# Performance work log

Hardware: AMD Instinct MI355X
Metric: run time of the kernel (lower is better)

Reference implementation:

```python
import jax, jax.numpy as jnp
import numpy as np

K_NEIGHBORS = 5
EPS = 1e-12  # torch F.normalize eps


def _l2_normalize(x):
    n = jnp.linalg.norm(x, axis=-1, keepdims=True)
    return x / jnp.maximum(n, EPS)


def setup_inputs() -> dict:
    key = jax.random.key(0)
    k1, k2, k3, k4 = jax.random.split(key, 4)
    B, D = 256, 512
    N, A = 50000, 8
    return {
        "z_flowed": jax.random.normal(k1, (B, D), dtype=jnp.float32),
        "target_attrs": jax.random.randint(k2, (B, A), 0, 3, dtype=jnp.int32),
        "train_embeddings": jax.random.normal(k3, (N, D), dtype=jnp.float32),
        "train_attributes": jax.random.randint(k4, (N, A), 0, 3, dtype=jnp.int32),
    }


def reference(z_flowed, target_attrs, train_embeddings, train_attributes):
    B = z_flowed.shape[0]
    A = target_attrs.shape[1]
    z_norm = _l2_normalize(z_flowed)          # [B, D]
    train_norm = _l2_normalize(train_embeddings)  # [N, D]

    # batched attribute match: [B, N] count of matching attributes
    match_score = (train_attributes[None, :, :] == target_attrs[:, None, :]).sum(-1)
    mask = (match_score >= (A - 1)).astype(z_norm.dtype)  # [B, N]

    # cosine similarities for all samples in one GEMM: [B, N]
    sims = jnp.einsum('nd,bd->bn', train_norm, z_norm)
    masked_sim = sims * mask

    top_k_values, _ = jax.lax.top_k(masked_sim, K_NEIGHBORS)  # [B, K]
    per_sample_loss = (1.0 - top_k_values).mean(-1)           # [B]

    # samples with fewer than k matching neighbors are skipped in the sum
    valid = (mask.sum(-1) >= K_NEIGHBORS).astype(per_sample_loss.dtype)
    return (per_sample_loss * valid).sum() / B
```

## Files before the change

### kernel.cpp

```cpp
#include <hip/hip_runtime.h>
#include <math.h>


constexpr int D = 512;
constexpr int A = 8;
constexpr int K_NEI = 5;
constexpr int SLOTS = 512;

__device__ __forceinline__ float wave_reduce_add(float v) {
    #pragma unroll
    for (int m = 1; m < 64; m <<= 1) v += __shfl_xor(v, m, 64);
    return v;
}

__global__ __launch_bounds__(64) void prep_kernel(
    const float* __restrict__ z, const int* __restrict__ tattr,
    float* __restrict__ z_norm, unsigned* __restrict__ tpacked,
    int* __restrict__ counters)
{
    const int b = blockIdx.x;
    const int lane = threadIdx.x;
    const float4* zrow = (const float4*)(z + (size_t)b * D);
    float4 v0 = zrow[lane * 2 + 0];
    float4 v1 = zrow[lane * 2 + 1];
    float ss = v0.x*v0.x + v0.y*v0.y + v0.z*v0.z + v0.w*v0.w
             + v1.x*v1.x + v1.y*v1.y + v1.z*v1.z + v1.w*v1.w;
    ss = wave_reduce_add(ss);
    const float scale = 1.0f / fmaxf(sqrtf(ss), 1e-12f);
    v0.x *= scale; v0.y *= scale; v0.z *= scale; v0.w *= scale;
    v1.x *= scale; v1.y *= scale; v1.z *= scale; v1.w *= scale;
    float4* orow = (float4*)(z_norm + (size_t)b * D);
    orow[lane * 2 + 0] = v0;
    orow[lane * 2 + 1] = v1;
    if (lane == 0) {
        unsigned p = 0;
        #pragma unroll
        for (int a = 0; a < A; a++)
            p |= ((unsigned)tattr[b * A + a] & 0xFu) << (4 * a);
        tpacked[b] = p;
        counters[b] = 0;
    }
}

__global__ __launch_bounds__(64) void scatter_kernel(
    const float* __restrict__ train, const int* __restrict__ trattr,
    const float* __restrict__ z_norm, const unsigned* __restrict__ tpacked,
    int* __restrict__ counters, float* __restrict__ simbuf)
{
    const int n = blockIdx.x;
    const int lane = threadIdx.x;

    const int* arow = trattr + (size_t)n * A;
    unsigned p = 0;
    #pragma unroll
    for (int a = 0; a < A; a++)
        p |= ((unsigned)arow[a] & 0xFu) << (4 * a);

    unsigned matchbits = 0;
    #pragma unroll
    for (int j = 0; j < 4; j++) {
        const int b = lane * 4 + j;
        const unsigned y = p ^ tpacked[b];
        const unsigned nz = (y | (y >> 1) | (y >> 2) | (y >> 3)) & 0x11111111u;
        if (__popc(nz) <= 1) matchbits |= (1u << j);
    }
    const unsigned long long any = __ballot(matchbits != 0);
    if (any == 0ULL) return;

    const float4* row4 = (const float4*)(train + (size_t)n * D);
    const float4 r0 = row4[lane * 2 + 0];
    const float4 r1 = row4[lane * 2 + 1];
    float ss = r0.x*r0.x + r0.y*r0.y + r0.z*r0.z + r0.w*r0.w
             + r1.x*r1.x + r1.y*r1.y + r1.z*r1.z + r1.w*r1.w;
    ss = wave_reduce_add(ss);
    const float inv_norm = 1.0f / fmaxf(sqrtf(ss), 1e-12f);

    #pragma unroll
    for (int j = 0; j < 4; j++) {
        unsigned long long bm = __ballot((matchbits >> j) & 1u);
        while (bm) {
            const int l = __ffsll((unsigned long long)bm) - 1;
            bm &= bm - 1;
            const int b = l * 4 + j;
            const float4* zr = (const float4*)(z_norm + (size_t)b * D);
            const float4 z0 = zr[lane * 2 + 0];
            const float4 z1 = zr[lane * 2 + 1];
            float d = r0.x*z0.x + r0.y*z0.y + r0.z*z0.z + r0.w*z0.w
                    + r1.x*z1.x + r1.y*z1.y + r1.z*z1.z + r1.w*z1.w;
            d = wave_reduce_add(d);
            if (lane == 0) {
                const float sim = d * inv_norm;
                const int idx = atomicAdd(&counters[b], 1);
                if (idx < SLOTS) simbuf[(size_t)b * SLOTS + idx] = sim;
            }
        }
    }
}

__global__ __launch_bounds__(256) void finalize_kernel(
    const int* __restrict__ counters, const float* __restrict__ simbuf,
    float* __restrict__ out, int Bt)
{
    const int b = threadIdx.x;
    const int cnt = counters[b];
    const int m = cnt < SLOTS ? cnt : SLOTS;
    float top[K_NEI];
    #pragma unroll
    for (int k = 0; k < K_NEI; k++) top[k] = -1e30f;
    const float* buf = simbuf + (size_t)b * SLOTS;
    for (int i = 0; i < m; i++) {
        const float v = buf[i];
        if (v > top[K_NEI - 1]) {
            top[K_NEI - 1] = v;
            #pragma unroll
            for (int k = K_NEI - 1; k > 0; k--) {
                if (top[k] > top[k - 1]) { float t = top[k]; top[k] = top[k - 1]; top[k - 1] = t; }
            }
        }
    }
    float s = 0.0f;
    #pragma unroll
    for (int k = 0; k < K_NEI; k++) s += fmaxf(top[k], 0.0f);
    float contrib = (cnt >= K_NEI) ? (1.0f - s * (1.0f / K_NEI)) : 0.0f;

    contrib = wave_reduce_add(contrib);
    __shared__ float part[4];
    const int wave = threadIdx.x >> 6;
    if ((threadIdx.x & 63) == 0) part[wave] = contrib;
    __syncthreads();
    if (threadIdx.x == 0)
        out[0] = (part[0] + part[1] + part[2] + part[3]) / (float)Bt;
}

extern "C" void kernel_launch(void* const* d_in, const int* in_sizes, int n_in,
                              void* d_out, int out_size, void* d_ws, size_t ws_size,
                              hipStream_t stream)
{
    const float* z      = (const float*)d_in[0];
    const int*   tattr  = (const int*)d_in[1];
    const float* train  = (const float*)d_in[2];
    const int*   trattr = (const int*)d_in[3];
    float* out = (float*)d_out;

    const int B = in_sizes[0] / D;
    const int N = in_sizes[2] / D;

    char* ws = (char*)d_ws;
    float*    z_norm   = (float*)ws;                        ws += (size_t)B * D * sizeof(float);
    unsigned* tpacked  = (unsigned*)ws;                     ws += (size_t)B * sizeof(unsigned);
    int*      counters = (int*)ws;                          ws += (size_t)B * sizeof(int);
    float*    simbuf   = (float*)ws;

    prep_kernel<<<B, 64, 0, stream>>>(z, tattr, z_norm, tpacked, counters);
    scatter_kernel<<<N, 64, 0, stream>>>(train, trattr, z_norm, tpacked, counters, simbuf);
    finalize_kernel<<<1, 256, 0, stream>>>(counters, simbuf, out, B);
}
```

Baseline: 205.9 us.

## Split sparse match into compaction, pair-parallel dot, and wave-parallel top-k

Replaces the one-block-per-train-row scatter kernel with a match kernel that compacts matching (row, query) pairs into a global list through LDS, then a persistent dot kernel that processes one pair per wave. Top-k becomes a wave-parallel selection per query, and counters are padded to separate cache lines to cut atomic contention. This is meant to remove the cost of launching 50000 tiny blocks, most of which exit early, and to balance the dot-product work across waves. In exchange it adds an extra kernel launch, global pair-buffer traffic and redundant reloads of train rows and their norms for each matching pair. It also silently drops pairs beyond fixed caps.

```diff
diff --git a/kernel.cpp b/kernel.cpp
--- a/kernel.cpp
+++ b/kernel.cpp
@@ -6,6 +6,9 @@
 constexpr int A = 8;
 constexpr int K_NEI = 5;
 constexpr int SLOTS = 512;
+constexpr int CSTRIDE = 16;
+constexpr int PAIR_CAP = 65536;
+constexpr int LDS_PAIR_CAP = 1024;
 
 __device__ __forceinline__ float wave_reduce_add(float v) {
     #pragma unroll
@@ -16,7 +19,8 @@
 __global__ __launch_bounds__(64) void prep_kernel(
     const float* __restrict__ z, const int* __restrict__ tattr,
     float* __restrict__ z_norm, unsigned* __restrict__ tpacked,
-    int* __restrict__ counters)
+    int* __restrict__ counters, int* __restrict__ npairs,
+    float* __restrict__ out)
 {
     const int b = blockIdx.x;
     const int lane = threadIdx.x;
@@ -38,98 +42,144 @@
         for (int a = 0; a < A; a++)
             p |= ((unsigned)tattr[b * A + a] & 0xFu) << (4 * a);
         tpacked[b] = p;
-        counters[b] = 0;
-    }
-}
-
-__global__ __launch_bounds__(64) void scatter_kernel(
-    const float* __restrict__ train, const int* __restrict__ trattr,
-    const float* __restrict__ z_norm, const unsigned* __restrict__ tpacked,
+        counters[b * CSTRIDE] = 0;
+        if (b == 0) { *npairs = 0; out[0] = 0.0f; }
+    }
+}
+
+__global__ __launch_bounds__(256) void match_kernel(
+    const int* __restrict__ trattr, const unsigned* __restrict__ tpacked,
+    unsigned* __restrict__ pairs, int* __restrict__ npairs, int N)
+{
+    __shared__ unsigned s_tp[256];
+    __shared__ unsigned s_pairs[LDS_PAIR_CAP];
+    __shared__ int s_cnt, s_base;
+
+    const int tid = threadIdx.x;
+    const int n = blockIdx.x * 256 + tid;
+    s_tp[tid] = tpacked[tid];
+    if (tid == 0) s_cnt = 0;
+    __syncthreads();
+
+    unsigned p = 0;
+    if (n < N) {
+        const int4* a4 = (const int4*)(trattr + (size_t)n * A);
+        const int4 x = a4[0], y = a4[1];
+        p  = ((unsigned)x.x & 0xFu)       | (((unsigned)x.y & 0xFu) << 4)
+           | (((unsigned)x.z & 0xFu) << 8)  | (((unsigned)x.w & 0xFu) << 12)
+           | (((unsigned)y.x & 0xFu) << 16) | (((unsigned)y.y & 0xFu) << 20)
+           | (((unsigned)y.z & 0xFu) << 24) | (((unsigned)y.w & 0xFu) << 28);
+    }
+
+    if (n < N) {
+        const uint4* tp4 = (const uint4*)s_tp;
+        #pragma unroll 4
+        for (int bq = 0; bq < 64; bq++) {
+            const uint4 t = tp4[bq];
+            #pragma unroll
+            for (int j = 0; j < 4; j++) {
+                const unsigned tv = (j == 0) ? t.x : (j == 1) ? t.y : (j == 2) ? t.z : t.w;
+                const unsigned yv = p ^ tv;
+                const unsigned nzhi = ((((yv & 0x77777777u) + 0x77777777u) | yv) & 0x88888888u);
+                if (__popc(nzhi) <= 1) {
+                    const int idx = atomicAdd(&s_cnt, 1);
+                    const unsigned pr = ((unsigned)n << 8) | (unsigned)(bq * 4 + j);
+                    if (idx < LDS_PAIR_CAP) s_pairs[idx] = pr;
+                }
+            }
+        }
+    }
+    __syncthreads();
+    const int cnt = min(s_cnt, LDS_PAIR_CAP);
+    if (tid == 0) s_base = atomicAdd(npairs, cnt);
+    __syncthreads();
+    const int base = s_base;
+    for (int i = tid; i < cnt; i += 256)
+        if (base + i < PAIR_CAP) pairs[base + i] = s_pairs[i];
+}
+
+__global__ __launch_bounds__(256) void dot_kernel(
+    const float* __restrict__ train, const float* __restrict__ z_norm,
+    const unsigned* __restrict__ pairs, const int* __restrict__ npairs,
     int* __restrict__ counters, float* __restrict__ simbuf)
 {
-    const int n = blockIdx.x;
-    const int lane = threadIdx.x;
-
-    const int* arow = trattr + (size_t)n * A;
-    unsigned p = 0;
-    #pragma unroll
-    for (int a = 0; a < A; a++)
-        p |= ((unsigned)arow[a] & 0xFu) << (4 * a);
-
-    unsigned matchbits = 0;
-    #pragma unroll
-    for (int j = 0; j < 4; j++) {
-        const int b = lane * 4 + j;
-        const unsigned y = p ^ tpacked[b];
-        const unsigned nz = (y | (y >> 1) | (y >> 2) | (y >> 3)) & 0x11111111u;
-        if (__popc(nz) <= 1) matchbits |= (1u << j);
-    }
-    const unsigned long long any = __ballot(matchbits != 0);
-    if (any == 0ULL) return;
-
-    const float4* row4 = (const float4*)(train + (size_t)n * D);
-    const float4 r0 = row4[lane * 2 + 0];
-    const float4 r1 = row4[lane * 2 + 1];
-    float ss = r0.x*r0.x + r0.y*r0.y + r0.z*r0.z + r0.w*r0.w
-             + r1.x*r1.x + r1.y*r1.y + r1.z*r1.z + r1.w*r1.w;
-    ss = wave_reduce_add(ss);
-    const float inv_norm = 1.0f / fmaxf(sqrtf(ss), 1e-12f);
-
-    #pragma unroll
-    for (int j = 0; j < 4; j++) {
-        unsigned long long bm = __ballot((matchbits >> j) & 1u);
-        while (bm) {
-            const int l = __ffsll((unsigned long long)bm) - 1;
-            bm &= bm - 1;
-            const int b = l * 4 + j;
-            const float4* zr = (const float4*)(z_norm + (size_t)b * D);
-            const float4 z0 = zr[lane * 2 + 0];
-            const float4 z1 = zr[lane * 2 + 1];
-            float d = r0.x*z0.x + r0.y*z0.y + r0.z*z0.z + r0.w*z0.w
-                    + r1.x*z1.x + r1.y*z1.y + r1.z*z1.z + r1.w*z1.w;
-            d = wave_reduce_add(d);
-            if (lane == 0) {
-                const float sim = d * inv_norm;
-                const int idx = atomicAdd(&counters[b], 1);
-                if (idx < SLOTS) simbuf[(size_t)b * SLOTS + idx] = sim;
-            }
-        }
-    }
-}
-
-__global__ __launch_bounds__(256) void finalize_kernel(
+    const int lane = threadIdx.x & 63;
+    const int w = blockIdx.x * 4 + (threadIdx.x >> 6);
+    const int nwaves = gridDim.x * 4;
+    const int np = min(*npairs, PAIR_CAP);
+
+    for (int i = w; i < np; i += nwaves) {
+        const unsigned pr = pairs[i];
+        const int n = (int)(pr >> 8);
+        const int b = (int)(pr & 255u);
+        const float4* row4 = (const float4*)(train + (size_t)n * D);
+        const float4* zr4  = (const float4*)(z_norm + (size_t)b * D);
+        const float4 r0 = row4[lane * 2 + 0];
+        const float4 r1 = row4[lane * 2 + 1];
+        const float4 z0 = zr4[lane * 2 + 0];
+        const float4 z1 = zr4[lane * 2 + 1];
+        float ss = r0.x*r0.x + r0.y*r0.y + r0.z*r0.z + r0.w*r0.w
+                 + r1.x*r1.x + r1.y*r1.y + r1.z*r1.z + r1.w*r1.w;
+        float dd = r0.x*z0.x + r0.y*z0.y + r0.z*z0.z + r0.w*z0.w
+                 + r1.x*z1.x + r1.y*z1.y + r1.z*z1.z + r1.w*z1.w;
+        #pragma unroll
+        for (int m = 1; m < 64; m <<= 1) {
+            ss += __shfl_xor(ss, m, 64);
+            dd += __shfl_xor(dd, m, 64);
+        }
+        if (lane == 0) {
+            const float sim = dd / fmaxf(sqrtf(ss), 1e-12f);
+            const int idx = atomicAdd(&counters[b * CSTRIDE], 1);
+            if (idx < SLOTS) simbuf[(size_t)b * SLOTS + idx] = sim;
+        }
+    }
+}
+
+__global__ __launch_bounds__(64) void topk_kernel(
     const int* __restrict__ counters, const float* __restrict__ simbuf,
     float* __restrict__ out, int Bt)
 {
-    const int b = threadIdx.x;
-    const int cnt = counters[b];
-    const int m = cnt < SLOTS ? cnt : SLOTS;
-    float top[K_NEI];
+    const int b = blockIdx.x;
+    const int lane = threadIdx.x;
+    const int cnt = counters[b * CSTRIDE];
+    const int m = min(cnt, SLOTS);
+    const float* buf = simbuf + (size_t)b * SLOTS;
+
+    float v[8];
     #pragma unroll
-    for (int k = 0; k < K_NEI; k++) top[k] = -1e30f;
-    const float* buf = simbuf + (size_t)b * SLOTS;
-    for (int i = 0; i < m; i++) {
-        const float v = buf[i];
-        if (v > top[K_NEI - 1]) {
-            top[K_NEI - 1] = v;
-            #pragma unroll
-            for (int k = K_NEI - 1; k > 0; k--) {
-                if (top[k] > top[k - 1]) { float t = top[k]; top[k] = top[k - 1]; top[k - 1] = t; }
-            }
-        }
-    }
+    for (int k = 0; k < 8; k++) {
+        const int i = lane + k * 64;
+        v[k] = (i < m) ? buf[i] : -1e30f;
+    }
+
     float s = 0.0f;
     #pragma unroll
-    for (int k = 0; k < K_NEI; k++) s += fmaxf(top[k], 0.0f);
-    float contrib = (cnt >= K_NEI) ? (1.0f - s * (1.0f / K_NEI)) : 0.0f;
-
-    contrib = wave_reduce_add(contrib);
-    __shared__ float part[4];
-    const int wave = threadIdx.x >> 6;
-    if ((threadIdx.x & 63) == 0) part[wave] = contrib;
-    __syncthreads();
-    if (threadIdx.x == 0)
-        out[0] = (part[0] + part[1] + part[2] + part[3]) / (float)Bt;
+    for (int r = 0; r < K_NEI; r++) {
+        float best = v[0];
+        #pragma unroll
+        for (int k = 1; k < 8; k++) best = fmaxf(best, v[k]);
+        float M = best;
+        #pragma unroll
+        for (int mm = 1; mm < 64; mm <<= 1) M = fmaxf(M, __shfl_xor(M, mm, 64));
+        s += fmaxf(M, 0.0f);
+        const unsigned long long bal = __ballot(best == M);
+        const int first = __ffsll(bal) - 1;
+        if (lane == first) {
+            if      (v[0] == M) v[0] = -1e30f;
+            else if (v[1] == M) v[1] = -1e30f;
+            else if (v[2] == M) v[2] = -1e30f;
+            else if (v[3] == M) v[3] = -1e30f;
+            else if (v[4] == M) v[4] = -1e30f;
+            else if (v[5] == M) v[5] = -1e30f;
+            else if (v[6] == M) v[6] = -1e30f;
+            else                v[7] = -1e30f;
+        }
+    }
+
+    if (lane == 0) {
+        const float contrib = (cnt >= K_NEI) ? (1.0f - s * (1.0f / K_NEI)) : 0.0f;
+        atomicAdd(out, contrib / (float)Bt);
+    }
 }
 
 extern "C" void kernel_launch(void* const* d_in, const int* in_sizes, int n_in,
@@ -146,12 +196,15 @@
     const int N = in_sizes[2] / D;
 
     char* ws = (char*)d_ws;
-    float*    z_norm   = (float*)ws;                        ws += (size_t)B * D * sizeof(float);
-    unsigned* tpacked  = (unsigned*)ws;                     ws += (size_t)B * sizeof(unsigned);
-    int*      counters = (int*)ws;                          ws += (size_t)B * sizeof(int);
-    float*    simbuf   = (float*)ws;
-
-    prep_kernel<<<B, 64, 0, stream>>>(z, tattr, z_norm, tpacked, counters);
-    scatter_kernel<<<N, 64, 0, stream>>>(train, trattr, z_norm, tpacked, counters, simbuf);
-    finalize_kernel<<<1, 256, 0, stream>>>(counters, simbuf, out, B);
-}
+    float*    z_norm   = (float*)ws;   ws += (size_t)B * D * sizeof(float);
+    unsigned* tpacked  = (unsigned*)ws; ws += (size_t)B * sizeof(unsigned);
+    int*      counters = (int*)ws;     ws += (size_t)B * CSTRIDE * sizeof(int);
+    float*    simbuf   = (float*)ws;   ws += (size_t)B * SLOTS * sizeof(float);
+    int*      npairs   = (int*)ws;     ws += 64;
+    unsigned* pairs    = (unsigned*)ws;
+
+    prep_kernel<<<B, 64, 0, stream>>>(z, tattr, z_norm, tpacked, counters, npairs, out);
+    match_kernel<<<(N + 255) / 256, 256, 0, stream>>>(trattr, tpacked, pairs, npairs, N);
+    dot_kernel<<<1024, 256, 0, stream>>>(train, z_norm, pairs, npairs, counters, simbuf);
+    topk_kernel<<<B, 64, 0, stream>>>(counters, simbuf, out, B);
+}
```

Measured after the change: 181.4 us. -11.9%, faster.
